# Kernel optimization log

Measured on AMD Instinct MI355X. Metric: run time of the kernel, lower is better.

The kernel has to match this reference:

```python
import jax, jax.numpy as jnp
import numpy as np

N_HEADS = 16
D_MODEL = 1024
D_K = D_MODEL // N_HEADS


def setup_inputs() -> dict:
    key = jax.random.key(0)
    ks = jax.random.split(key, 7)
    b, n = 4, 2048
    s = 0.02  # keep projections well-scaled
    return {
        "Q": jax.random.normal(ks[0], (b, n, D_MODEL), jnp.float32),
        "K": jax.random.normal(ks[1], (b, n, D_MODEL), jnp.float32),
        "V": jax.random.normal(ks[2], (b, n, D_MODEL), jnp.float32),
        "w_q": jax.random.normal(ks[3], (D_MODEL, D_MODEL), jnp.float32) * s,
        "w_k": jax.random.normal(ks[4], (D_MODEL, D_MODEL), jnp.float32) * s,
        "w_v": jax.random.normal(ks[5], (D_MODEL, D_MODEL), jnp.float32) * s,
        "w_o": jax.random.normal(ks[6], (D_MODEL, D_MODEL), jnp.float32) * s,
    }


def reference(Q, K, V, w_q, w_k, w_v, w_o):
    b, n, _ = Q.shape
    # nn.Linear(x) = x @ W.T ; weights stored [out, in]
    q = (Q @ w_q.T).reshape(b, n, N_HEADS, D_K).transpose(0, 2, 1, 3)  # [b,h,n,dk]
    k = (K @ w_k.T).reshape(b, n, N_HEADS, D_K).transpose(0, 2, 1, 3)
    v = (V @ w_v.T).reshape(b, n, N_HEADS, D_K).transpose(0, 2, 1, 3)
    scores = jnp.einsum("bhqd,bhkd->bhqk", q, k) / jnp.sqrt(jnp.float32(D_K))
    causal = jnp.tril(jnp.ones((n, n), dtype=bool))  # keep lower triangle incl. diag
    scores = jnp.where(causal[None, None], scores, -jnp.inf)
    weights = jax.nn.softmax(scores, axis=-1)
    attn = jnp.einsum("bhqk,bhkd->bhqd", weights, v)
    attn = attn.transpose(0, 2, 1, 3).reshape(b, n, D_MODEL)
    return attn @ w_o.T
```

## Files before the change

kernel.cpp:

```cpp
#include <hip/hip_runtime.h>
#include <hip/hip_bf16.h>
#include <cstdint>
#include <cstddef>


typedef __bf16 bf16_t;
typedef bf16_t bf16x4 __attribute__((ext_vector_type(4)));
typedef bf16_t bf16x8 __attribute__((ext_vector_type(8)));
typedef float floatx4 __attribute__((ext_vector_type(4)));

#define MFMA(a, b, c) __builtin_amdgcn_mfma_f32_16x16x32_bf16((a), (b), (c), 0, 0, 0)
#define NEG_BIG (-30000.0f)

static __device__ __forceinline__ bf16_t f2bf(float x) { return (bf16_t)x; }

static __device__ __forceinline__ bf16x8 cvt8p(const floatx4 a, const floatx4 b) {
  bf16x8 r;
  r[0] = (bf16_t)a[0]; r[1] = (bf16_t)a[1]; r[2] = (bf16_t)a[2]; r[3] = (bf16_t)a[3];
  r[4] = (bf16_t)b[0]; r[5] = (bf16_t)b[1]; r[6] = (bf16_t)b[2]; r[7] = (bf16_t)b[3];
  return r;
}

static __device__ __forceinline__ void g2l16(const void* g, void* l) {
  __builtin_amdgcn_global_load_lds(
      (const __attribute__((address_space(1))) void*)g,
      (__attribute__((address_space(3))) void*)l, 16, 0, 0);
}

__global__ void detect_dtype(const unsigned short* __restrict__ w,
                             int* __restrict__ flag) {
  const unsigned short u = w[threadIdx.x];
  const bool big = (u & 0x7F80u) >= 0x3F80u;
  const unsigned long long m = __ballot(big);
  if (threadIdx.x == 0) *flag = (m != 0ull) ? 1 : 0;
}

__global__ __launch_bounds__(256)
void cvt_w_swz(const void* __restrict__ s0, const void* __restrict__ s1,
               const void* __restrict__ s2, bf16_t* __restrict__ dst,
               const int* __restrict__ flag)
{
  const void* src = blockIdx.y == 0 ? s0 : (blockIdx.y == 1 ? s1 : s2);
  bf16_t* d = dst + (size_t)blockIdx.y * (1024 * 1024);
  const int i    = blockIdx.x * 256 + threadIdx.x;
  const int row  = i >> 7;
  const int col0 = (i & 127) * 8;
  const int dcol = col0 ^ ((row & 6) << 2);
  bf16x8 v;
  if (*flag) {
    const float* s = (const float*)src + (size_t)row * 1024 + col0;
    v = cvt8p(*(const floatx4*)s, *(const floatx4*)(s + 4));
  } else {
    v = *(const bf16x8*)((const bf16_t*)src + (size_t)row * 1024 + col0);
  }
  *(bf16x8*)(d + (size_t)row * 1024 + dcol) = v;
}

static __device__ __forceinline__ void gemm_tile_map(int& bm, int& bn) {
  const int f  = (int)(blockIdx.y * gridDim.x + blockIdx.x);
  const int xj = f & 7, sq = f >> 3;
  bm = ((xj << 3) | (sq >> 3)) * 128;
  bn = (sq & 7) * 128;
}

static __device__ __forceinline__ void gemm_tile_map64(int& bm, int& bn) {
  const int f  = (int)(blockIdx.y * gridDim.x + blockIdx.x);
  const int xj = f & 7, sq = f >> 3;
  bm = ((xj << 4) | (sq >> 3)) * 64;
  bn = (sq & 7) * 128;
}

template <bool AF32, typename OutT>
static __device__ __forceinline__
void gemm_rs_core(const void* __restrict__ Av, const bf16_t* __restrict__ W,
                  OutT* __restrict__ C,
                  bf16_t (*sA)[128 * 40], bf16_t (*sB)[128 * 32])
{
  const int K = 1024;
  const int tid  = threadIdx.x;
  const int wave = tid >> 6;
  const int lane = tid & 63;
  const int wm = wave >> 1, wn = wave & 1;
  int bm, bn;
  gemm_tile_map(bm, bn);
  const int quad = lane >> 4, r16 = lane & 15;
  const int cW = (quad * 8) ^ ((r16 & 6) << 2);

  floatx4 acc[4][4];
  #pragma unroll
  for (int i = 0; i < 4; ++i)
    #pragma unroll
    for (int j = 0; j < 4; ++j) acc[i][j] = {0.f, 0.f, 0.f, 0.f};

  const int srow = tid >> 2;
  const int scol = (tid & 3) * 8;
  const size_t a0 = (size_t)(bm + srow) * K + scol;
  const size_t a1 = a0 + (size_t)64 * K;

  const int ch0 = wave * 2;
  const int r0  = lane >> 2;
  const int ce  = (lane & 3) * 8;
  const bf16_t* Wg0 = W + (size_t)(bn + ch0 * 16 + r0) * K + ce;
  const bf16_t* Wg1 = Wg0 + (size_t)16 * K;

  floatx4 fa[2][2];
  bf16x8  ba[2];
  auto stageA = [&](int k0) {
    if constexpr (AF32) {
      const float* Af = (const float*)Av;
      fa[0][0] = *(const floatx4*)(Af + a0 + k0);
      fa[0][1] = *(const floatx4*)(Af + a0 + k0 + 4);
      fa[1][0] = *(const floatx4*)(Af + a1 + k0);
      fa[1][1] = *(const floatx4*)(Af + a1 + k0 + 4);
    } else {
      const bf16_t* Ab = (const bf16_t*)Av;
      ba[0] = *(const bf16x8*)(Ab + a0 + k0);
      ba[1] = *(const bf16x8*)(Ab + a1 + k0);
    }
  };

  stageA(0);
  g2l16(Wg0, &sB[0][ch0 * 512]);
  g2l16(Wg1, &sB[0][(ch0 + 1) * 512]);

  for (int t = 0; t < 32; ++t) {
    const int buf = t & 1;
    {
      bf16x8 va0, va1;
      if constexpr (AF32) { va0 = cvt8p(fa[0][0], fa[0][1]); va1 = cvt8p(fa[1][0], fa[1][1]); }
      else                { va0 = ba[0]; va1 = ba[1]; }
      *(bf16x8*)&sA[buf][srow * 40 + scol]        = va0;
      *(bf16x8*)&sA[buf][(srow + 64) * 40 + scol] = va1;
    }
    __syncthreads();
    if (t + 1 < 32) {
      const int k0 = (t + 1) * 32;
      g2l16(Wg0 + k0, &sB[buf ^ 1][ch0 * 512]);
      g2l16(Wg1 + k0, &sB[buf ^ 1][(ch0 + 1) * 512]);
      stageA(k0);
    }

    bf16x8 af[4], bv[4];
    #pragma unroll
    for (int mi = 0; mi < 4; ++mi)
      af[mi] = *(const bf16x8*)&sA[buf][(wm * 64 + mi * 16 + r16) * 40 + quad * 8];
    #pragma unroll
    for (int ni = 0; ni < 4; ++ni)
      bv[ni] = *(const bf16x8*)&sB[buf][(wn * 64 + ni * 16 + r16) * 32 + cW];
    #pragma unroll
    for (int mi = 0; mi < 4; ++mi)
      #pragma unroll
      for (int ni = 0; ni < 4; ++ni)
        acc[mi][ni] = MFMA(af[mi], bv[ni], acc[mi][ni]);
  }

  #pragma unroll
  for (int mi = 0; mi < 4; ++mi)
    #pragma unroll
    for (int ni = 0; ni < 4; ++ni)
      #pragma unroll
      for (int r = 0; r < 4; ++r) {
        const int row = bm + wm * 64 + mi * 16 + quad * 4 + r;
        const int col = bn + wn * 64 + ni * 16 + r16;
        C[(size_t)row * 1024 + col] = (OutT)acc[mi][ni][r];
      }
}

template <typename OutT>
__global__ __launch_bounds__(256, 3)
void gemm_rs(const void* __restrict__ A0, const void* __restrict__ A1,
             const void* __restrict__ A2, const bf16_t* __restrict__ Wb,
             OutT* __restrict__ C0, OutT* __restrict__ C1,
             OutT* __restrict__ C2, const int* __restrict__ flag)
{
  __shared__ __align__(16) bf16_t sA[2][128 * 40];
  __shared__ __align__(16) bf16_t sB[2][128 * 32];
  const int z = blockIdx.z;
  const void*   A = z == 0 ? A0 : (z == 1 ? A1 : A2);
  const bf16_t* W = Wb + (size_t)z * (1024 * 1024);
  OutT*         C = z == 0 ? C0 : (z == 1 ? C1 : C2);
  if (*flag) gemm_rs_core<true,  OutT>(A, W, C, sA, sB);
  else       gemm_rs_core<false, OutT>(A, W, C, sA, sB);
}

__global__ __launch_bounds__(256, 4)
void gemm_o(const bf16_t* __restrict__ A, const bf16_t* __restrict__ W,
            float* __restrict__ C)
{
  const int K = 1024;
  __shared__ __align__(16) bf16_t sA[2][64 * 40];
  __shared__ __align__(16) bf16_t sB[2][128 * 32];
  const int tid  = threadIdx.x;
  const int wave = tid >> 6;
  const int lane = tid & 63;
  int bm, bn;
  gemm_tile_map64(bm, bn);
  const int quad = lane >> 4, r16 = lane & 15;
  const int cW = (quad * 8) ^ ((r16 & 6) << 2);

  floatx4 acc[4][2];
  #pragma unroll
  for (int i = 0; i < 4; ++i)
    #pragma unroll
    for (int j = 0; j < 2; ++j) acc[i][j] = {0.f, 0.f, 0.f, 0.f};

  const int srow = tid >> 2;
  const int scol = (tid & 3) * 8;
  const size_t a0 = (size_t)(bm + srow) * K + scol;

  const int ch0 = wave * 2;
  const int r0  = lane >> 2;
  const int ce  = (lane & 3) * 8;
  const bf16_t* Wg0 = W + (size_t)(bn + ch0 * 16 + r0) * K + ce;
  const bf16_t* Wg1 = Wg0 + (size_t)16 * K;

  bf16x8 ba;
  auto stageA = [&](int k0) { ba = *(const bf16x8*)(A + a0 + k0); };

  stageA(0);
  g2l16(Wg0, &sB[0][ch0 * 512]);
  g2l16(Wg1, &sB[0][(ch0 + 1) * 512]);

  for (int t = 0; t < 32; ++t) {
    const int buf = t & 1;
    *(bf16x8*)&sA[buf][srow * 40 + scol] = ba;
    __syncthreads();
    if (t + 1 < 32) {
      const int k0 = (t + 1) * 32;
      g2l16(Wg0 + k0, &sB[buf ^ 1][ch0 * 512]);
      g2l16(Wg1 + k0, &sB[buf ^ 1][(ch0 + 1) * 512]);
      stageA(k0);
    }

    bf16x8 af[4], bv[2];
    #pragma unroll
    for (int mi = 0; mi < 4; ++mi)
      af[mi] = *(const bf16x8*)&sA[buf][(mi * 16 + r16) * 40 + quad * 8];
    #pragma unroll
    for (int ni = 0; ni < 2; ++ni)
      bv[ni] = *(const bf16x8*)&sB[buf][(wave * 32 + ni * 16 + r16) * 32 + cW];
    #pragma unroll
    for (int mi = 0; mi < 4; ++mi)
      #pragma unroll
      for (int ni = 0; ni < 2; ++ni)
        acc[mi][ni] = MFMA(af[mi], bv[ni], acc[mi][ni]);
  }

  #pragma unroll
  for (int mi = 0; mi < 4; ++mi)
    #pragma unroll
    for (int ni = 0; ni < 2; ++ni)
      #pragma unroll
      for (int r = 0; r < 4; ++r) {
        const int row = bm + mi * 16 + quad * 4 + r;
        const int col = bn + wave * 32 + ni * 16 + r16;
        C[(size_t)row * 1024 + col] = acc[mi][ni][r];
      }
}

__global__ __launch_bounds__(256, 4)
void flash_attn(bf16_t* qio, const bf16_t* __restrict__ kh,
                const bf16_t* __restrict__ vh)
{
  __shared__ __align__(16) bf16_t sK[64 * 64];
  __shared__ __align__(16) bf16_t sVt[64 * 64];
  __shared__ __align__(16) bf16_t sP[64 * 64];
  const int tid  = threadIdx.x;
  const int wave = tid >> 6;
  const int lane = tid & 63;
  const int quad = lane >> 4, r16 = lane & 15;

  const int f  = (int)(blockIdx.y * gridDim.x + blockIdx.x);
  const int xj = f & 7, sq = f >> 3;
  const int bh = xj + (sq >> 5) * 8;
  const int q0 = (31 - (sq & 31)) * 64;
  const int b = bh >> 4, h = bh & 15;
  const size_t hb = ((size_t)b * 2048) * 1024 + (size_t)h * 64;
  const int swl = (r16 & 7) << 3;

  bf16x8 qf[2];
  #pragma unroll
  for (int ks = 0; ks < 2; ++ks)
    qf[ks] = *(const bf16x8*)(qio + hb +
        (size_t)(q0 + wave * 16 + r16) * 1024 + ks * 32 + quad * 8);

  floatx4 o[4];
  #pragma unroll
  for (int nd = 0; nd < 4; ++nd) o[nd] = {0.f, 0.f, 0.f, 0.f};
  float mrow = NEG_BIG, lrow = 0.f;

  const float sc = 0.125f * 1.44269504089f;
  const int kend = q0 + 64;
  const int qrow = q0 + wave * 16 + r16;

  bf16x8 kst[2], vst[2];
  #pragma unroll
  for (int j = 0; j < 2; ++j) {
    const int c = j * 256 + tid;
    kst[j] = *(const bf16x8*)(kh + hb + (size_t)(c >> 3) * 1024 + (c & 7) * 8);
    vst[j] = *(const bf16x8*)(vh + hb + (size_t)(c & 63) * 1024 + (c >> 6) * 8);
  }

  for (int kv0 = 0; kv0 < kend; kv0 += 64) {
    #pragma unroll
    for (int j = 0; j < 2; ++j) {
      const int c = j * 256 + tid;
      const int krow = c >> 3, kcol = (c & 7) * 8;
      *(bf16x8*)&sK[krow * 64 + (kcol ^ ((krow & 7) << 3))] = kst[j];
      const int vkv = c & 63, vd = (c >> 6) * 8;
      #pragma unroll
      for (int e = 0; e < 8; ++e)
        sVt[(vd + e) * 64 + (vkv ^ (e << 3))] = vst[j][e];
    }
    __syncthreads();

    if (kv0 + 64 < kend) {
      #pragma unroll
      for (int j = 0; j < 2; ++j) {
        const int c = j * 256 + tid;
        kst[j] = *(const bf16x8*)(kh + hb + (size_t)(kv0 + 64 + (c >> 3)) * 1024 + (c & 7) * 8);
        vst[j] = *(const bf16x8*)(vh + hb + (size_t)(kv0 + 64 + (c & 63)) * 1024 + (c >> 6) * 8);
      }
    }

    floatx4 st[4];
    #pragma unroll
    for (int nk = 0; nk < 4; ++nk) st[nk] = {0.f, 0.f, 0.f, 0.f};
    #pragma unroll
    for (int ks = 0; ks < 2; ++ks) {
      bf16x8 bk[4];
      #pragma unroll
      for (int nk = 0; nk < 4; ++nk)
        bk[nk] = *(const bf16x8*)&sK[(nk * 16 + r16) * 64 + ((ks * 32 + quad * 8) ^ swl)];
      #pragma unroll
      for (int nk = 0; nk < 4; ++nk)
        st[nk] = MFMA(bk[nk], qf[ks], st[nk]);
    }

    const bool domask = (kv0 + 63 > q0 + wave * 16);
    #pragma unroll
    for (int nk = 0; nk < 4; ++nk)
      #pragma unroll
      for (int r = 0; r < 4; ++r) {
        float t = st[nk][r] * sc;
        if (domask && (kv0 + nk * 16 + quad * 4 + r > qrow)) t = NEG_BIG;
        st[nk][r] = t;
      }

    float mx = fmaxf(fmaxf(st[0][0], st[0][1]), fmaxf(st[0][2], st[0][3]));
    #pragma unroll
    for (int nk = 1; nk < 4; ++nk)
      mx = fmaxf(mx, fmaxf(fmaxf(st[nk][0], st[nk][1]),
                           fmaxf(st[nk][2], st[nk][3])));
    mx = fmaxf(mx, __shfl_xor(mx, 16, 64));
    mx = fmaxf(mx, __shfl_xor(mx, 32, 64));

    if (!__all(mx <= mrow)) {
      const float mnew  = fmaxf(mrow, mx);
      const float alpha = exp2f(mrow - mnew);
      mrow = mnew;
      lrow *= alpha;
      #pragma unroll
      for (int r = 0; r < 4; ++r) {
        const float ar = __shfl(alpha, quad * 4 + r, 64);
        #pragma unroll
        for (int nd = 0; nd < 4; ++nd) o[nd][r] *= ar;
      }
    }

    float ls = 0.f;
    #pragma unroll
    for (int nk = 0; nk < 4; ++nk) {
      bf16x4 pk;
      #pragma unroll
      for (int r = 0; r < 4; ++r) {
        const bf16_t pb = f2bf(exp2f(st[nk][r] - mrow));
        ls += (float)pb;
        pk[r] = pb;
      }
      *(bf16x4*)&sP[(wave * 16 + r16) * 64 + ((nk * 16 + quad * 4) ^ swl)] = pk;
    }
    ls += __shfl_xor(ls, 16, 64);
    ls += __shfl_xor(ls, 32, 64);
    lrow += ls;
    __syncthreads();

    #pragma unroll
    for (int ks = 0; ks < 2; ++ks) {
      const int cb = (ks * 32 + quad * 8) ^ swl;
      const bf16x8 pa = *(const bf16x8*)&sP[(wave * 16 + r16) * 64 + cb];
      bf16x8 vb[4];
      #pragma unroll
      for (int nd = 0; nd < 4; ++nd)
        vb[nd] = *(const bf16x8*)&sVt[(nd * 16 + r16) * 64 + cb];
      #pragma unroll
      for (int nd = 0; nd < 4; ++nd)
        o[nd] = MFMA(pa, vb[nd], o[nd]);
    }
    __syncthreads();
  }

  #pragma unroll
  for (int r = 0; r < 4; ++r) {
    const float lr  = __shfl(lrow, quad * 4 + r, 64);
    const float inv = 1.f / lr;
    const int row = q0 + wave * 16 + quad * 4 + r;
    #pragma unroll
    for (int nd = 0; nd < 4; ++nd)
      qio[hb + (size_t)row * 1024 + nd * 16 + r16] = f2bf(o[nd][r] * inv);
  }
}

extern "C" void kernel_launch(void* const* d_in, const int* in_sizes, int n_in,
                              void* d_out, int out_size, void* d_ws, size_t ws_size,
                              hipStream_t stream) {
  (void)in_sizes; (void)n_in; (void)out_size; (void)ws_size;
  const size_t TSZ = (size_t)8192 * 1024;
  int*    flag = (int*)d_ws;
  bf16_t* qws  = (bf16_t*)((char*)d_ws + 16);
  bf16_t* kws  = qws + TSZ;
  bf16_t* vws  = (bf16_t*)d_out;
  bf16_t* wsl  = (bf16_t*)d_out + TSZ;

  detect_dtype<<<1, 64, 0, stream>>>((const unsigned short*)d_in[3], flag);

  cvt_w_swz<<<dim3(512, 3), 256, 0, stream>>>(d_in[3], d_in[4], d_in[5], wsl, flag);

  gemm_rs<bf16_t><<<dim3(8, 64, 3), 256, 0, stream>>>(
      d_in[0], d_in[1], d_in[2], wsl, qws, kws, vws, flag);

  flash_attn<<<dim3(64, 32), 256, 0, stream>>>(qws, kws, vws);

  cvt_w_swz<<<dim3(512, 1), 256, 0, stream>>>(d_in[6], d_in[6], d_in[6], kws, flag);

  gemm_o<<<dim3(8, 128), 256, 0, stream>>>(qws, kws, (float*)d_out);
}
```

Measured before the change: 396.1 us.

## Enlarge flash attention query tile to 128 rows with 8 waves

The flash attention kernel now uses 512 threads (8 waves) per block, each block handling 128 query rows instead of 64. Each K/V tile loaded into shared memory is therefore reused by twice as many query rows, which cuts global K/V traffic and loop overhead. Block-to-tile mapping now alternates query order between groups to balance the causal workload. The GEMM loops also issue the A-operand global load before the async weight loads. A larger block raises per-block shared memory and register pressure and halves the number of blocks.

```diff
diff --git a/kernel.cpp b/kernel.cpp
--- a/kernel.cpp
+++ b/kernel.cpp
@@ -135,9 +135,9 @@
     __syncthreads();
     if (t + 1 < 32) {
       const int k0 = (t + 1) * 32;
+      stageA(k0);
       g2l16(Wg0 + k0, &sB[buf ^ 1][ch0 * 512]);
       g2l16(Wg1 + k0, &sB[buf ^ 1][(ch0 + 1) * 512]);
-      stageA(k0);
     }
 
     bf16x8 af[4], bv[4];
@@ -227,9 +227,9 @@
     __syncthreads();
     if (t + 1 < 32) {
       const int k0 = (t + 1) * 32;
+      stageA(k0);
       g2l16(Wg0 + k0, &sB[buf ^ 1][ch0 * 512]);
       g2l16(Wg1 + k0, &sB[buf ^ 1][(ch0 + 1) * 512]);
-      stageA(k0);
     }
 
     bf16x8 af[4], bv[2];
@@ -258,22 +258,26 @@
       }
 }
 
-__global__ __launch_bounds__(256, 4)
+__global__ __launch_bounds__(512, 4)
 void flash_attn(bf16_t* qio, const bf16_t* __restrict__ kh,
                 const bf16_t* __restrict__ vh)
 {
   __shared__ __align__(16) bf16_t sK[64 * 64];
   __shared__ __align__(16) bf16_t sVt[64 * 64];
-  __shared__ __align__(16) bf16_t sP[64 * 64];
+  __shared__ __align__(16) bf16_t sP[128 * 64];
   const int tid  = threadIdx.x;
   const int wave = tid >> 6;
   const int lane = tid & 63;
   const int quad = lane >> 4, r16 = lane & 15;
 
-  const int f  = (int)(blockIdx.y * gridDim.x + blockIdx.x);
-  const int xj = f & 7, sq = f >> 3;
-  const int bh = xj + (sq >> 5) * 8;
-  const int q0 = (31 - (sq & 31)) * 64;
+  const int f   = (int)(blockIdx.y * gridDim.x + blockIdx.x);
+  const int xj  = f & 7, s = f >> 3;
+  const int k   = s >> 5, cc = s & 31;
+  const int bhi = k * 2 + (cc >> 4);
+  const int q4  = cc & 15;
+  const int qidx = (k & 1) ? 15 - q4 : q4;
+  const int bh  = xj + bhi * 8;
+  const int q0  = qidx * 128;
   const int b = bh >> 4, h = bh & 15;
   const size_t hb = ((size_t)b * 2048) * 1024 + (size_t)h * 64;
   const int swl = (r16 & 7) << 3;
@@ -290,37 +294,27 @@
   float mrow = NEG_BIG, lrow = 0.f;
 
   const float sc = 0.125f * 1.44269504089f;
-  const int kend = q0 + 64;
+  const int kend = q0 + 128;
   const int qrow = q0 + wave * 16 + r16;
 
-  bf16x8 kst[2], vst[2];
-  #pragma unroll
-  for (int j = 0; j < 2; ++j) {
-    const int c = j * 256 + tid;
-    kst[j] = *(const bf16x8*)(kh + hb + (size_t)(c >> 3) * 1024 + (c & 7) * 8);
-    vst[j] = *(const bf16x8*)(vh + hb + (size_t)(c & 63) * 1024 + (c >> 6) * 8);
-  }
+  bf16x8 kst, vst;
+  kst = *(const bf16x8*)(kh + hb + (size_t)(tid >> 3) * 1024 + (tid & 7) * 8);
+  vst = *(const bf16x8*)(vh + hb + (size_t)(tid & 63) * 1024 + (tid >> 6) * 8);
 
   for (int kv0 = 0; kv0 < kend; kv0 += 64) {
-    #pragma unroll
-    for (int j = 0; j < 2; ++j) {
-      const int c = j * 256 + tid;
-      const int krow = c >> 3, kcol = (c & 7) * 8;
-      *(bf16x8*)&sK[krow * 64 + (kcol ^ ((krow & 7) << 3))] = kst[j];
-      const int vkv = c & 63, vd = (c >> 6) * 8;
+    {
+      const int krow = tid >> 3, kcol = (tid & 7) * 8;
+      *(bf16x8*)&sK[krow * 64 + (kcol ^ ((krow & 7) << 3))] = kst;
+      const int vkv = tid & 63, vd = (tid >> 6) * 8;
       #pragma unroll
       for (int e = 0; e < 8; ++e)
-        sVt[(vd + e) * 64 + (vkv ^ (e << 3))] = vst[j][e];
+        sVt[(vd + e) * 64 + (vkv ^ (e << 3))] = vst[e];
     }
     __syncthreads();
 
     if (kv0 + 64 < kend) {
-      #pragma unroll
-      for (int j = 0; j < 2; ++j) {
-        const int c = j * 256 + tid;
-        kst[j] = *(const bf16x8*)(kh + hb + (size_t)(kv0 + 64 + (c >> 3)) * 1024 + (c & 7) * 8);
-        vst[j] = *(const bf16x8*)(vh + hb + (size_t)(kv0 + 64 + (c & 63)) * 1024 + (c >> 6) * 8);
-      }
+      kst = *(const bf16x8*)(kh + hb + (size_t)(kv0 + 64 + (tid >> 3)) * 1024 + (tid & 7) * 8);
+      vst = *(const bf16x8*)(vh + hb + (size_t)(kv0 + 64 + (tid & 63)) * 1024 + (tid >> 6) * 8);
     }
 
     floatx4 st[4];
@@ -429,7 +423,7 @@
   gemm_rs<bf16_t><<<dim3(8, 64, 3), 256, 0, stream>>>(
       d_in[0], d_in[1], d_in[2], wsl, qws, kws, vws, flag);
 
-  flash_attn<<<dim3(64, 32), 256, 0, stream>>>(qws, kws, vws);
+  flash_attn<<<dim3(8, 128), 512, 0, stream>>>(qws, kws, vws);
 
   cvt_w_swz<<<dim3(512, 1), 256, 0, stream>>>(d_in[6], d_in[6], d_in[6], kws, flag);
 
```

Result: slower. 404.5 us (+2.1%).
